# Optimization experiments

Measured on AMD Instinct MI355X. Metric: run time of the kernel, lower is better.

The kernel has to match this reference:

```python
import jax, jax.numpy as jnp
import numpy as np

N = 3                      # data qubits (wires 1,2,3)
ANC = 0                    # ancilla wire
DATA = [1, 2, 3]
HAD = jnp.array([[1.0, 1.0], [1.0, -1.0]], jnp.float32) * np.float32(1.0 / np.sqrt(2.0))


def ry_mat(theta):
    c, s = jnp.cos(theta / 2), jnp.sin(theta / 2)
    return jnp.stack([jnp.stack([c, -s]), jnp.stack([s, c])])


def cry_mat(theta):
    # 4x4 controlled-RY in |ctrl,tgt> basis: block-diag(I2, RY)
    U = jnp.zeros((4, 4), jnp.float32)
    U = U.at[:2, :2].set(jnp.eye(2, dtype=jnp.float32))
    return U.at[2:, 2:].set(ry_mat(theta))


def apply_1q(state, U, w):
    # state: [B,2,2,2,2]; wire w lives on axis w+1
    st = jnp.moveaxis(state, w + 1, -1)
    st = st @ U.T
    return jnp.moveaxis(st, -1, w + 1)


def apply_2q(state, U4, w1, w2):
    U = U4.reshape(2, 2, 2, 2)  # [out1,out2,in1,in2]
    st = jnp.moveaxis(state, (w1 + 1, w2 + 1), (-2, -1))
    st = jnp.einsum('abij,...ij->...ab', U, st)
    return jnp.moveaxis(st, (-2, -1), (w1 + 1, w2 + 1))


def phase_flip(state, wire_bits):
    # multiply amplitude by -1 where each (wire, bit) matches.
    # This is exactly the X-sandwiched multi-controlled-Z of the source.
    idx = [slice(None)] * 5
    for w, b in wire_bits:
        idx[w + 1] = b
    return state.at[tuple(idx)].multiply(-1.0)


def circuit(x, theta_fo, theta_ado):
    # AmplitudeEmbedding(normalize=True) on data wires; ancilla in |0>
    xn = x / jnp.linalg.norm(x, axis=1, keepdims=True)
    B = x.shape[0]
    data = xn.reshape(B, 2, 2, 2)                        # wires 1,2,3 (wire 1 MSB)
    state = jnp.stack([data, jnp.zeros_like(data)], axis=1)  # [B, anc, w1, w2, w3]

    # Flexible oracle: RY(t) on ancilla, bitstring-controlled phase flip, RY(-t)
    for b in range(2 ** N):
        bits = [(b >> (N - 1 - i)) & 1 for i in range(N)]
        state = apply_1q(state, ry_mat(theta_fo[b]), ANC)
        state = phase_flip(state, [(ANC, 1)] + list(zip(DATA, bits)))
        state = apply_1q(state, ry_mat(-theta_fo[b]), ANC)

    # ADO with Pauli-X sandwich
    for w in DATA:
        state = apply_1q(state, HAD, w)
    for i in range(N):
        state = apply_2q(state, cry_mat(theta_ado[i]), DATA[i], DATA[(i + 1) % N])
    # X-sandwiched MCZ on data wires == phase flip where all data wires are 0
    state = phase_flip(state, [(w, 0) for w in DATA])
    for i in range(N):
        state = apply_2q(state, cry_mat(theta_ado[i + N]), DATA[i], DATA[(i + 1) % N])
    for w in DATA:
        state = apply_1q(state, HAD, w)

    # <PauliZ> on last data wire (axis 4): P(bit=0) - P(bit=1)
    probs = state * state
    return probs[..., 0].sum(axis=(1, 2, 3)) - probs[..., 1].sum(axis=(1, 2, 3))


def setup_inputs() -> dict:
    key = jax.random.key(0)
    k1, k2, k3 = jax.random.split(key, 3)
    B = 1048576
    x_batch = jax.random.normal(k1, (B, 2 ** N), dtype=jnp.float32)
    theta_fo = jax.random.uniform(k2, (2 ** N,), jnp.float32, -np.pi, np.pi)
    theta_ado = 0.1 * jax.random.normal(k3, (2 * N,), dtype=jnp.float32)
    return {"x_batch": x_batch, "theta_fo": theta_fo, "theta_ado": theta_ado}


def reference(x_batch, theta_fo, theta_ado):
    return circuit(x_batch, theta_fo, theta_ado)
```

## Files before the change

### kernel.cpp

```cpp
#include <hip/hip_runtime.h>
#include <math.h>


#define RSQRT2 0.70710678118654752440f

#define HAD(m) do {                                               \
    _Pragma("unroll")                                             \
    for (int idx = 0; idx < 16; ++idx) {                          \
      if (!(idx & (m))) {                                         \
        float a_ = st[idx], b_ = st[idx | (m)];                   \
        st[idx]       = (a_ + b_) * RSQRT2;                       \
        st[idx | (m)] = (a_ - b_) * RSQRT2;                       \
      }                                                           \
    }                                                             \
  } while (0)

#define CRY(cm, tm, cc, ss) do {                                  \
    _Pragma("unroll")                                             \
    for (int idx = 0; idx < 16; ++idx) {                          \
      if ((idx & (cm)) && !(idx & (tm))) {                        \
        float a_ = st[idx], b_ = st[idx | (tm)];                  \
        st[idx]        = (cc) * a_ - (ss) * b_;                   \
        st[idx | (tm)] = (ss) * a_ + (cc) * b_;                   \
      }                                                           \
    }                                                             \
  } while (0)

__global__ __launch_bounds__(256) void gqhan_kernel(
    const float* __restrict__ x,
    const float* __restrict__ theta_fo,
    const float* __restrict__ theta_ado,
    float* __restrict__ out, int B)
{
  __shared__ float cf[8], sf[8];
  __shared__ float ca[6], sa[6];
  int t = threadIdx.x;
  if (t < 8) {
    float th = theta_fo[t];
    cf[t] = cosf(th);
    sf[t] = sinf(th);
  } else if (t < 14) {
    float th = 0.5f * theta_ado[t - 8];
    ca[t - 8] = cosf(th);
    sa[t - 8] = sinf(th);
  }
  __syncthreads();

  int i = blockIdx.x * blockDim.x + threadIdx.x;
  if (i >= B) return;

  const float4* xp = (const float4*)(x + (size_t)i * 8u);
  float4 lo = xp[0], hi = xp[1];
  float v[8] = {lo.x, lo.y, lo.z, lo.w, hi.x, hi.y, hi.z, hi.w};

  float n2 = 0.0f;
#pragma unroll
  for (int k = 0; k < 8; ++k) n2 = fmaf(v[k], v[k], n2);

  float st[16];
#pragma unroll
  for (int b = 0; b < 8; ++b) {
    st[b]     =  cf[b] * v[b];
    st[8 + b] = -sf[b] * v[b];
  }

  HAD(4); HAD(2); HAD(1);

  CRY(4, 2, ca[0], sa[0]);
  CRY(2, 1, ca[1], sa[1]);
  CRY(1, 4, ca[2], sa[2]);

  st[0] = -st[0];
  st[8] = -st[8];

  CRY(4, 2, ca[3], sa[3]);
  CRY(2, 1, ca[4], sa[4]);
  CRY(1, 4, ca[5], sa[5]);

  float r = 0.0f;
#pragma unroll
  for (int idx = 0; idx < 16; idx += 2)
    r = fmaf(st[idx], st[idx | 1], r);
  r = r + r;

  out[i] = r * __builtin_amdgcn_rcpf(n2);
}

extern "C" void kernel_launch(void* const* d_in, const int* in_sizes, int n_in,
                              void* d_out, int out_size, void* d_ws, size_t ws_size,
                              hipStream_t stream) {
  const float* x         = (const float*)d_in[0];
  const float* theta_fo  = (const float*)d_in[1];
  const float* theta_ado = (const float*)d_in[2];
  float* out = (float*)d_out;
  int B = in_sizes[0] / 8;
  int block = 256;
  int grid = (B + block - 1) / block;
  gqhan_kernel<<<grid, block, 0, stream>>>(x, theta_fo, theta_ado, out, B);
}
```

Before: 79.91 us.

## Collapse circuit into precomputed 8x8 quadratic form evaluated per sample

Adds a tiny setup kernel that folds the oracle rotations and the fixed ADO gate sequence into an 8x8 matrix M, so the expectation becomes v^T M v / |v|^2. The main kernel now does a 64-FMA quadratic form with M loaded from workspace instead of simulating the 16-amplitude state gate by gate. The goal is to cut per-sample arithmetic and shared-memory setup. It adds a second kernel launch and a dependency on workspace memory.

```diff
diff --git a/kernel.cpp b/kernel.cpp
--- a/kernel.cpp
+++ b/kernel.cpp
@@ -4,48 +4,79 @@
 
 #define RSQRT2 0.70710678118654752440f
 
-#define HAD(m) do {                                               \
+#define HAD8(y, m) do {                                           \
     _Pragma("unroll")                                             \
-    for (int idx = 0; idx < 16; ++idx) {                          \
-      if (!(idx & (m))) {                                         \
-        float a_ = st[idx], b_ = st[idx | (m)];                   \
-        st[idx]       = (a_ + b_) * RSQRT2;                       \
-        st[idx | (m)] = (a_ - b_) * RSQRT2;                       \
+    for (int e = 0; e < 8; ++e) {                                 \
+      if (!(e & (m))) {                                           \
+        float a_ = y[e], b_ = y[e | (m)];                         \
+        y[e]       = (a_ + b_) * RSQRT2;                          \
+        y[e | (m)] = (a_ - b_) * RSQRT2;                          \
       }                                                           \
     }                                                             \
   } while (0)
 
-#define CRY(cm, tm, cc, ss) do {                                  \
+#define CRY8(y, cm, tm, cc, ss) do {                              \
     _Pragma("unroll")                                             \
-    for (int idx = 0; idx < 16; ++idx) {                          \
-      if ((idx & (cm)) && !(idx & (tm))) {                        \
-        float a_ = st[idx], b_ = st[idx | (tm)];                  \
-        st[idx]        = (cc) * a_ - (ss) * b_;                   \
-        st[idx | (tm)] = (ss) * a_ + (cc) * b_;                   \
+    for (int e = 0; e < 8; ++e) {                                 \
+      if ((e & (cm)) && !(e & (tm))) {                            \
+        float a_ = y[e], b_ = y[e | (tm)];                        \
+        y[e]        = (cc) * a_ - (ss) * b_;                      \
+        y[e | (tm)] = (ss) * a_ + (cc) * b_;                      \
       }                                                           \
     }                                                             \
   } while (0)
 
-__global__ __launch_bounds__(256) void gqhan_kernel(
-    const float* __restrict__ x,
+#define ADO8(y) do {                                              \
+    HAD8(y, 4); HAD8(y, 2); HAD8(y, 1);                           \
+    CRY8(y, 4, 2, ca[0], sa[0]);                                  \
+    CRY8(y, 2, 1, ca[1], sa[1]);                                  \
+    CRY8(y, 1, 4, ca[2], sa[2]);                                  \
+    y[0] = -y[0];                                                 \
+    CRY8(y, 4, 2, ca[3], sa[3]);                                  \
+    CRY8(y, 2, 1, ca[4], sa[4]);                                  \
+    CRY8(y, 1, 4, ca[5], sa[5]);                                  \
+  } while (0)
+
+__global__ __launch_bounds__(64) void gqhan_setup(
     const float* __restrict__ theta_fo,
     const float* __restrict__ theta_ado,
+    float* __restrict__ Mout)
+{
+  int t = threadIdx.x;
+  int j = t >> 3, k = t & 7;
+
+  float ca[6], sa[6];
+#pragma unroll
+  for (int q = 0; q < 6; ++q) {
+    float th = 0.5f * theta_ado[q];
+    ca[q] = cosf(th);
+    sa[q] = sinf(th);
+  }
+
+  float yj[8], yk[8];
+#pragma unroll
+  for (int e = 0; e < 8; ++e) {
+    yj[e] = (e == j) ? 1.0f : 0.0f;
+    yk[e] = (e == k) ? 1.0f : 0.0f;
+  }
+  ADO8(yj);
+  ADO8(yk);
+
+  float m = 0.0f;
+#pragma unroll
+  for (int e = 0; e < 8; e += 2)
+    m += yj[e] * yk[e + 1] + yj[e + 1] * yk[e];
+
+  float tj = theta_fo[j], tk = theta_fo[k];
+  float w = cosf(tj) * cosf(tk) + sinf(tj) * sinf(tk);
+  Mout[t] = m * w;
+}
+
+__global__ __launch_bounds__(256) void gqhan_main(
+    const float* __restrict__ x,
+    const float* __restrict__ M,
     float* __restrict__ out, int B)
 {
-  __shared__ float cf[8], sf[8];
-  __shared__ float ca[6], sa[6];
-  int t = threadIdx.x;
-  if (t < 8) {
-    float th = theta_fo[t];
-    cf[t] = cosf(th);
-    sf[t] = sinf(th);
-  } else if (t < 14) {
-    float th = 0.5f * theta_ado[t - 8];
-    ca[t - 8] = cosf(th);
-    sa[t - 8] = sinf(th);
-  }
-  __syncthreads();
-
   int i = blockIdx.x * blockDim.x + threadIdx.x;
   if (i >= B) return;
 
@@ -55,33 +86,25 @@
 
   float n2 = 0.0f;
 #pragma unroll
-  for (int k = 0; k < 8; ++k) n2 = fmaf(v[k], v[k], n2);
+  for (int q = 0; q < 8; ++q) n2 = fmaf(v[q], v[q], n2);
 
-  float st[16];
-#pragma unroll
-  for (int b = 0; b < 8; ++b) {
-    st[b]     =  cf[b] * v[b];
-    st[8 + b] = -sf[b] * v[b];
-  }
-
-  HAD(4); HAD(2); HAD(1);
-
-  CRY(4, 2, ca[0], sa[0]);
-  CRY(2, 1, ca[1], sa[1]);
-  CRY(1, 4, ca[2], sa[2]);
-
-  st[0] = -st[0];
-  st[8] = -st[8];
-
-  CRY(4, 2, ca[3], sa[3]);
-  CRY(2, 1, ca[4], sa[4]);
-  CRY(1, 4, ca[5], sa[5]);
-
+  const float4* __restrict__ M4 = (const float4*)M;
   float r = 0.0f;
 #pragma unroll
-  for (int idx = 0; idx < 16; idx += 2)
-    r = fmaf(st[idx], st[idx | 1], r);
-  r = r + r;
+  for (int row = 0; row < 8; ++row) {
+    float4 m0 = M4[2 * row + 0];
+    float4 m1 = M4[2 * row + 1];
+    float y;
+    y = m0.x * v[0];
+    y = fmaf(m0.y, v[1], y);
+    y = fmaf(m0.z, v[2], y);
+    y = fmaf(m0.w, v[3], y);
+    y = fmaf(m1.x, v[4], y);
+    y = fmaf(m1.y, v[5], y);
+    y = fmaf(m1.z, v[6], y);
+    y = fmaf(m1.w, v[7], y);
+    r = fmaf(v[row], y, r);
+  }
 
   out[i] = r * __builtin_amdgcn_rcpf(n2);
 }
@@ -93,8 +116,12 @@
   const float* theta_fo  = (const float*)d_in[1];
   const float* theta_ado = (const float*)d_in[2];
   float* out = (float*)d_out;
+  float* M   = (float*)d_ws;
   int B = in_sizes[0] / 8;
+
+  gqhan_setup<<<1, 64, 0, stream>>>(theta_fo, theta_ado, M);
+
   int block = 256;
   int grid = (B + block - 1) / block;
-  gqhan_kernel<<<grid, block, 0, stream>>>(x, theta_fo, theta_ado, out, B);
+  gqhan_main<<<grid, block, 0, stream>>>(x, M, out, B);
 }
```

Result: no change. 79.41 us (-0.6%).
